# Kernel optimization log

Hardware: AMD Instinct MI355X
Metric: run time of the kernel (lower is better)

Reference implementation:

```python
import jax, jax.numpy as jnp
from jax import lax
import numpy as np

S, B, I, H, O = 65536, 1, 2, 128, 1


def setup_inputs() -> dict:
    key = jax.random.key(0)
    k1, k2, k3, k4 = jax.random.split(key, 4)
    # xavier_normal-style scales
    s_ih = (2.0 / (4 * H + I)) ** 0.5
    s_hh = (2.0 / (4 * H + H)) ** 0.5
    s_out = (2.0 / (H + O)) ** 0.5
    return {
        "x": jax.random.normal(k1, (S, B, I), jnp.float32),
        "h0": jnp.zeros((1, B, H), jnp.float32),
        "c0": jnp.zeros((1, B, H), jnp.float32),
        "W_ih": jax.random.normal(k2, (4 * H, I), jnp.float32) * s_ih,
        "W_hh": jax.random.normal(k3, (4 * H, H), jnp.float32) * s_hh,
        "b_ih": jnp.zeros((4 * H,), jnp.float32),
        "b_hh": jnp.zeros((4 * H,), jnp.float32),
        "W_out": jax.random.normal(k4, (O, H), jnp.float32) * s_out,
        "b_out": jnp.zeros((O,), jnp.float32),
    }


def reference(x, h0, c0, W_ih, W_hh, b_ih, b_hh, W_out, b_out):
    # Precompute input-to-gate projections for all timesteps: (S, B, 4H)
    xg = jnp.einsum("sbi,gi->sbg", x, W_ih) + b_ih + b_hh

    def step(carry, xg_t):
        h, c = carry  # (B, H) each
        gates = xg_t + h @ W_hh.T  # (B, 4H); PyTorch order i,f,g,o
        i, f, g, o = jnp.split(gates, 4, axis=-1)
        i = jax.nn.sigmoid(i)
        f = jax.nn.sigmoid(f)
        g = jnp.tanh(g)
        o = jax.nn.sigmoid(o)
        c = f * c + i * g
        h = o * jnp.tanh(c)
        return (h, c), h

    (_, _), hs = lax.scan(step, (h0[0], c0[0]), xg)  # hs: (S, B, H)
    out = jnp.tanh(hs.transpose(1, 0, 2))  # (B, S, H), matches permute(1,0,2)
    out = out @ W_out.T + b_out  # (B, S, O)
    return out.reshape(out.shape[0] * out.shape[1], -1)  # (B*S, O)
```

## Files before the change

kernel.cpp:

```cpp
#include <hip/hip_runtime.h>

#define S_LEN 65536
#define HDIM 128

typedef _Float16 half2_t __attribute__((ext_vector_type(2)));
typedef _Float16 half8_t __attribute__((ext_vector_type(8)));
typedef float f32x4 __attribute__((ext_vector_type(4)));

__device__ __forceinline__ float sigm(float x) {
    return 1.0f / (1.0f + __expf(-x));
}
__device__ __forceinline__ float tanh_fast(float x) {
    return 2.0f / (1.0f + __expf(-2.0f * x)) - 1.0f;
}
__device__ __forceinline__ float dot2(half2_t a, half2_t b, float c) {
#if __has_builtin(__builtin_amdgcn_fdot2)
    return __builtin_amdgcn_fdot2(a, b, c, false);
#else
    return fmaf((float)a.x, (float)b.x, fmaf((float)a.y, (float)b.y, c));
#endif
}

#define WG_BARRIER() do {                                         \
    asm volatile("s_waitcnt lgkmcnt(0)" ::: "memory");            \
    __builtin_amdgcn_s_barrier();                                 \
    asm volatile("" ::: "memory");                                \
} while (0)

__global__ __launch_bounds__(512)
__attribute__((amdgpu_waves_per_eu(2, 2)))
void lstm_seq_mfma(const float* __restrict__ x,
                   const float* __restrict__ h0,
                   const float* __restrict__ c0,
                   const float* __restrict__ W_ih,
                   const float* __restrict__ W_hh,
                   const float* __restrict__ b_ih,
                   const float* __restrict__ b_hh,
                   _Float16* __restrict__ h_hist)
{
    __shared__ __align__(16) _Float16 h_buf[2][HDIM];

    const int tid  = threadIdx.x;
    const int lane = tid & 63;
    const int w    = tid >> 6;
    const int m    = lane & 15;
    const int quad = lane >> 4;

#define LOAD_AF(i, cc) \
    half8_t af_##i##_##cc; { \
        const float* s_ = W_hh + (size_t)((i) * 128 + w * 16 + m) * HDIM \
                               + 32 * (cc) + 8 * quad; \
        af_##i##_##cc = (half8_t){ \
            (_Float16)s_[0], (_Float16)s_[1], (_Float16)s_[2], (_Float16)s_[3], \
            (_Float16)s_[4], (_Float16)s_[5], (_Float16)s_[6], (_Float16)s_[7] }; \
        asm volatile("" : "+v"(af_##i##_##cc)); }
    LOAD_AF(0, 0) LOAD_AF(0, 1) LOAD_AF(0, 2) LOAD_AF(0, 3)
    LOAD_AF(1, 0) LOAD_AF(1, 1) LOAD_AF(1, 2) LOAD_AF(1, 3)
    LOAD_AF(2, 0) LOAD_AF(2, 1) LOAD_AF(2, 2) LOAD_AF(2, 3)
    LOAD_AF(3, 0) LOAD_AF(3, 1) LOAD_AF(3, 2) LOAD_AF(3, 3)
#undef LOAD_AF

    const bool worker = (m < 4);
    const int  hidx   = w * 16 + quad * 4 + (m & 3);
    float wi00 = 0.f, wi01 = 0.f, bs0 = 0.f;
    float wi10 = 0.f, wi11 = 0.f, bs1 = 0.f;
    float wi20 = 0.f, wi21 = 0.f, bs2 = 0.f;
    float wi30 = 0.f, wi31 = 0.f, bs3 = 0.f;
    float c = 0.0f;
    if (worker) {
        const int r0 = hidx;
        const int r1 = hidx + 128;
        const int r2 = hidx + 256;
        const int r3 = hidx + 384;
        wi00 = W_ih[2 * r0]; wi01 = W_ih[2 * r0 + 1]; bs0 = b_ih[r0] + b_hh[r0];
        wi10 = W_ih[2 * r1]; wi11 = W_ih[2 * r1 + 1]; bs1 = b_ih[r1] + b_hh[r1];
        wi20 = W_ih[2 * r2]; wi21 = W_ih[2 * r2 + 1]; bs2 = b_ih[r2] + b_hh[r2];
        wi30 = W_ih[2 * r3]; wi31 = W_ih[2 * r3 + 1]; bs3 = b_ih[r3] + b_hh[r3];
        c = c0[hidx];
    }
    if (tid < HDIM) h_buf[0][tid] = (_Float16)h0[tid];
    __syncthreads();

    const float2* xp = (const float2*)x;
    float2 xcur = xp[0];
    float2 xn1  = xp[1];

    const bool selod = (m & 1) != 0;
    const bool selhi = (m & 2) != 0;

#define MFMA_T(i) \
    acc##i = __builtin_amdgcn_mfma_f32_16x16x32_f16(af_##i##_0, bf0, acc##i, 0, 0, 0); \
    acc##i = __builtin_amdgcn_mfma_f32_16x16x32_f16(af_##i##_1, bf1, acc##i, 0, 0, 0); \
    acc##i = __builtin_amdgcn_mfma_f32_16x16x32_f16(af_##i##_2, bf2, acc##i, 0, 0, 0); \
    acc##i = __builtin_amdgcn_mfma_f32_16x16x32_f16(af_##i##_3, bf3, acc##i, 0, 0, 0);

#define STEP(T, RB, WB) { \
     \
    const half8_t* hb_ = (const half8_t*)(RB); \
    half8_t bf0 = hb_[quad]; \
    half8_t bf1 = hb_[4 + quad]; \
    half8_t bf2 = hb_[8 + quad]; \
    half8_t bf3 = hb_[12 + quad]; \
    f32x4 acc0 = {0.f, 0.f, 0.f, 0.f}; \
    f32x4 acc1 = acc0, acc2 = acc0, acc3 = acc0; \
    MFMA_T(0) MFMA_T(1) MFMA_T(2) MFMA_T(3) \
    int tn_ = (T) + 2; if (tn_ >= S_LEN) tn_ = S_LEN - 1; \
    float2 xnew_ = xp[tn_]; \
    const float xg0 = fmaf(wi00, xcur.x, fmaf(wi01, xcur.y, bs0)); \
    const float xg1 = fmaf(wi10, xcur.x, fmaf(wi11, xcur.y, bs1)); \
    const float xg2 = fmaf(wi20, xcur.x, fmaf(wi21, xcur.y, bs2)); \
    const float xg3 = fmaf(wi30, xcur.x, fmaf(wi31, xcur.y, bs3)); \
    if (worker) { \
        float sa_, sb_; \
        sa_ = selod ? acc0[1] : acc0[0]; sb_ = selod ? acc0[3] : acc0[2]; \
        const float g0 = (selhi ? sb_ : sa_) + xg0; \
        sa_ = selod ? acc1[1] : acc1[0]; sb_ = selod ? acc1[3] : acc1[2]; \
        const float g1 = (selhi ? sb_ : sa_) + xg1; \
        sa_ = selod ? acc2[1] : acc2[0]; sb_ = selod ? acc2[3] : acc2[2]; \
        const float g2 = (selhi ? sb_ : sa_) + xg2; \
        sa_ = selod ? acc3[1] : acc3[0]; sb_ = selod ? acc3[3] : acc3[2]; \
        const float g3 = (selhi ? sb_ : sa_) + xg3; \
        const float gi = sigm(g0); \
        const float gf = sigm(g1); \
        const float gg = tanh_fast(g2); \
        const float go = sigm(g3); \
        c = fmaf(gf, c, gi * gg); \
        const float hv_ = go * tanh_fast(c); \
        const _Float16 hf_ = (_Float16)hv_; \
        (WB)[hidx] = hf_;                        \
        h_hist[(size_t)(T) * HDIM + hidx] = hf_;  \
    } \
    xcur = xn1; xn1 = xnew_; \
    WG_BARRIER(); }

    #pragma unroll 1
    for (int t = 0; t < S_LEN; t += 2) {
        STEP(t,     h_buf[0], h_buf[1])
        STEP(t + 1, h_buf[1], h_buf[0])
    }
#undef STEP
#undef MFMA_T
}

__global__ __launch_bounds__(256)
void out_proj(const _Float16* __restrict__ h_hist,
              const float* __restrict__ W_out,
              const float* __restrict__ b_out,
              float* __restrict__ out)
{
    const int lane  = threadIdx.x & 63;
    const int gwave = (blockIdx.x * 256 + threadIdx.x) >> 6;
    const int nwave = (gridDim.x * 256) >> 6;

    const float wo0 = W_out[2 * lane + 0];
    const float wo1 = W_out[2 * lane + 1];
    const float bout = b_out[0];

    for (int t = gwave; t < S_LEN; t += nwave) {
        half2_t hv = ((const half2_t*)(h_hist + t * HDIM))[lane];
        float p = tanh_fast((float)hv.x) * wo0 + tanh_fast((float)hv.y) * wo1;
        #pragma unroll
        for (int off = 32; off > 0; off >>= 1)
            p += __shfl_xor(p, off, 64);
        if (lane == 0) out[t] = p + bout;
    }
}

#define H_HI_OFF 144
__global__ __launch_bounds__(1024)
__attribute__((amdgpu_waves_per_eu(4, 4)))
void lstm_seq_full(const float* __restrict__ x,
                   const float* __restrict__ h0,
                   const float* __restrict__ c0,
                   const float* __restrict__ W_ih,
                   const float* __restrict__ W_hh,
                   const float* __restrict__ b_ih,
                   const float* __restrict__ b_hh,
                   const float* __restrict__ W_out,
                   const float* __restrict__ b_out,
                   float* __restrict__ out)
{
    __shared__ __align__(16) unsigned char h_raw[2 * H_HI_OFF];
    __shared__ float gates_part[2 * 512];
    __shared__ float red_sh[2];

    const int tid  = threadIdx.x;
    const int j    = tid >> 1;
    const int half = tid & 1;

    const float2* wr2 = (const float2*)(W_hh + j * HDIM + half * 64);
#define WDEF(i) half2_t W##i; { float2 t = wr2[i]; \
        W##i.x = (_Float16)t.x; W##i.y = (_Float16)t.y; } \
        asm volatile("" : "+v"(W##i));
    WDEF(0)  WDEF(1)  WDEF(2)  WDEF(3)  WDEF(4)  WDEF(5)  WDEF(6)  WDEF(7)
    WDEF(8)  WDEF(9)  WDEF(10) WDEF(11) WDEF(12) WDEF(13) WDEF(14) WDEF(15)
    WDEF(16) WDEF(17) WDEF(18) WDEF(19) WDEF(20) WDEF(21) WDEF(22) WDEF(23)
    WDEF(24) WDEF(25) WDEF(26) WDEF(27) WDEF(28) WDEF(29) WDEF(30) WDEF(31)
#undef WDEF

    float wih0 = 0.0f, wih1 = 0.0f, bias = 0.0f;
    if (half == 0) {
        wih0 = W_ih[2 * j + 0];
        wih1 = W_ih[2 * j + 1];
        bias = b_ih[j] + b_hh[j];
    }

    float c = 0.0f, wout = 0.0f;
    _Float16* hw = (_Float16*)(h_raw + ((tid < 64) ? 2 * tid
                                                   : H_HI_OFF + 2 * (tid - 64)));
    if (tid < HDIM) {
        c = c0[tid];
        wout = W_out[tid];
        *hw = (_Float16)h0[tid];
    }
    const float bout = b_out[0];
    __syncthreads();

    const float2* xp = (const float2*)x;
    float2 xcur = xp[0];
    const half8_t* hp = (const half8_t*)(h_raw + half * H_HI_OFF);

    #pragma unroll 1
    for (int t = 0; t < S_LEN; ++t) {
        const int tn = (t + 1 < S_LEN) ? (t + 1) : (S_LEN - 1);
        float2 xnext = xp[tn];

        float a0 = fmaf(wih0, xcur.x, fmaf(wih1, xcur.y, bias));
        float a1 = 0.0f, a2 = 0.0f, a3 = 0.0f;

#define CHUNK(cc, w0_, w1_, w2_, w3_) {                         \
        half8_t hv = hp[cc];                                    \
        half2_t p0 = { hv[0], hv[1] };                          \
        half2_t p1 = { hv[2], hv[3] };                          \
        half2_t p2 = { hv[4], hv[5] };                          \
        half2_t p3 = { hv[6], hv[7] };                          \
        a0 = dot2(w0_, p0, a0);                                 \
        a1 = dot2(w1_, p1, a1);                                 \
        a2 = dot2(w2_, p2, a2);                                 \
        a3 = dot2(w3_, p3, a3); }
        CHUNK(0, W0,  W1,  W2,  W3)
        CHUNK(1, W4,  W5,  W6,  W7)
        CHUNK(2, W8,  W9,  W10, W11)
        CHUNK(3, W12, W13, W14, W15)
        CHUNK(4, W16, W17, W18, W19)
        CHUNK(5, W20, W21, W22, W23)
        CHUNK(6, W24, W25, W26, W27)
        CHUNK(7, W28, W29, W30, W31)
#undef CHUNK

        gates_part[half * 512 + j] = (a0 + a1) + (a2 + a3);
        __syncthreads();

        if (tid < HDIM) {
            float gi = sigm(gates_part[tid]            + gates_part[tid + 512]);
            float gf = sigm(gates_part[tid + 128]      + gates_part[tid + 640]);
            float gg = tanh_fast(gates_part[tid + 256] + gates_part[tid + 768]);
            float go = sigm(gates_part[tid + 384]      + gates_part[tid + 896]);
            c = fmaf(gf, c, gi * gg);
            float h = go * tanh_fast(c);
            *hw = (_Float16)h;

            float p = tanh_fast(h) * wout;
            #pragma unroll
            for (int off = 32; off > 0; off >>= 1)
                p += __shfl_xor(p, off, 64);
            if ((tid & 63) == 0) red_sh[tid >> 6] = p;
        }
        __syncthreads();

        if (tid == 0) out[t] = red_sh[0] + red_sh[1] + bout;
        xcur = xnext;
    }
}

extern "C" void kernel_launch(void* const* d_in, const int* in_sizes, int n_in,
                              void* d_out, int out_size, void* d_ws, size_t ws_size,
                              hipStream_t stream) {
    const float* x     = (const float*)d_in[0];
    const float* h0    = (const float*)d_in[1];
    const float* c0    = (const float*)d_in[2];
    const float* W_ih  = (const float*)d_in[3];
    const float* W_hh  = (const float*)d_in[4];
    const float* b_ih  = (const float*)d_in[5];
    const float* b_hh  = (const float*)d_in[6];
    const float* W_out = (const float*)d_in[7];
    const float* b_out = (const float*)d_in[8];

    const size_t need = (size_t)S_LEN * HDIM * sizeof(_Float16);
    if (ws_size >= need) {
        _Float16* h_hist = (_Float16*)d_ws;
        lstm_seq_mfma<<<dim3(1), dim3(512), 0, stream>>>(
            x, h0, c0, W_ih, W_hh, b_ih, b_hh, h_hist);
        out_proj<<<dim3(1024), dim3(256), 0, stream>>>(
            h_hist, W_out, b_out, (float*)d_out);
    } else {
        lstm_seq_full<<<dim3(1), dim3(1024), 0, stream>>>(
            x, h0, c0, W_ih, W_hh, b_ih, b_hh, W_out, b_out, (float*)d_out);
    }
}
```

Before: 40.53 ms.

## Halve LSTM recurrence workgroup to four waves with two MFMA tiles each

The sequential LSTM kernel now runs with 256 threads (4 waves) instead of 512, and each wave computes two 16-row tiles per gate, holding twice as many W_hh fragments in registers. Gate selection picks among two tiles per gate, and eight lanes per 16 act as workers. Fewer waves should make the per-step workgroup barrier cheaper and cut cross-wave synchronization latency. The cost is twice the serial MFMA work and register pressure per wave. It also adds a pointer-increment history store and moves the x-projection FMAs ahead of the MFMAs.

```diff
diff --git a/kernel.cpp b/kernel.cpp
--- a/kernel.cpp
+++ b/kernel.cpp
@@ -27,8 +27,8 @@
     asm volatile("" ::: "memory");                                \
 } while (0)
 
-__global__ __launch_bounds__(512)
-__attribute__((amdgpu_waves_per_eu(2, 2)))
+__global__ __launch_bounds__(256)
+__attribute__((amdgpu_waves_per_eu(1, 1)))
 void lstm_seq_mfma(const float* __restrict__ x,
                    const float* __restrict__ h0,
                    const float* __restrict__ c0,
@@ -46,22 +46,26 @@
     const int m    = lane & 15;
     const int quad = lane >> 4;
 
-#define LOAD_AF(i, cc) \
-    half8_t af_##i##_##cc; { \
-        const float* s_ = W_hh + (size_t)((i) * 128 + w * 16 + m) * HDIM \
+#define LOAD_AF(i, ti, cc) \
+    half8_t af_##i##_##ti##_##cc; { \
+        const float* s_ = W_hh + (size_t)((i) * 128 + w * 32 + 16 * (ti) + m) * HDIM \
                                + 32 * (cc) + 8 * quad; \
-        af_##i##_##cc = (half8_t){ \
+        af_##i##_##ti##_##cc = (half8_t){ \
             (_Float16)s_[0], (_Float16)s_[1], (_Float16)s_[2], (_Float16)s_[3], \
             (_Float16)s_[4], (_Float16)s_[5], (_Float16)s_[6], (_Float16)s_[7] }; \
-        asm volatile("" : "+v"(af_##i##_##cc)); }
-    LOAD_AF(0, 0) LOAD_AF(0, 1) LOAD_AF(0, 2) LOAD_AF(0, 3)
-    LOAD_AF(1, 0) LOAD_AF(1, 1) LOAD_AF(1, 2) LOAD_AF(1, 3)
-    LOAD_AF(2, 0) LOAD_AF(2, 1) LOAD_AF(2, 2) LOAD_AF(2, 3)
-    LOAD_AF(3, 0) LOAD_AF(3, 1) LOAD_AF(3, 2) LOAD_AF(3, 3)
+        asm volatile("" : "+v"(af_##i##_##ti##_##cc)); }
+    LOAD_AF(0,0,0) LOAD_AF(0,0,1) LOAD_AF(0,0,2) LOAD_AF(0,0,3)
+    LOAD_AF(0,1,0) LOAD_AF(0,1,1) LOAD_AF(0,1,2) LOAD_AF(0,1,3)
+    LOAD_AF(1,0,0) LOAD_AF(1,0,1) LOAD_AF(1,0,2) LOAD_AF(1,0,3)
+    LOAD_AF(1,1,0) LOAD_AF(1,1,1) LOAD_AF(1,1,2) LOAD_AF(1,1,3)
+    LOAD_AF(2,0,0) LOAD_AF(2,0,1) LOAD_AF(2,0,2) LOAD_AF(2,0,3)
+    LOAD_AF(2,1,0) LOAD_AF(2,1,1) LOAD_AF(2,1,2) LOAD_AF(2,1,3)
+    LOAD_AF(3,0,0) LOAD_AF(3,0,1) LOAD_AF(3,0,2) LOAD_AF(3,0,3)
+    LOAD_AF(3,1,0) LOAD_AF(3,1,1) LOAD_AF(3,1,2) LOAD_AF(3,1,3)
 #undef LOAD_AF
 
-    const bool worker = (m < 4);
-    const int  hidx   = w * 16 + quad * 4 + (m & 3);
+    const bool worker = (m < 8);
+    const int  hidx   = w * 32 + 16 * ((m >> 2) & 1) + 4 * quad + (m & 3);
     float wi00 = 0.f, wi01 = 0.f, bs0 = 0.f;
     float wi10 = 0.f, wi11 = 0.f, bs1 = 0.f;
     float wi20 = 0.f, wi21 = 0.f, bs2 = 0.f;
@@ -87,39 +91,53 @@
 
     const bool selod = (m & 1) != 0;
     const bool selhi = (m & 2) != 0;
-
-#define MFMA_T(i) \
-    acc##i = __builtin_amdgcn_mfma_f32_16x16x32_f16(af_##i##_0, bf0, acc##i, 0, 0, 0); \
-    acc##i = __builtin_amdgcn_mfma_f32_16x16x32_f16(af_##i##_1, bf1, acc##i, 0, 0, 0); \
-    acc##i = __builtin_amdgcn_mfma_f32_16x16x32_f16(af_##i##_2, bf2, acc##i, 0, 0, 0); \
-    acc##i = __builtin_amdgcn_mfma_f32_16x16x32_f16(af_##i##_3, bf3, acc##i, 0, 0, 0);
-
-#define STEP(T, RB, WB) { \
+    const bool selti = (m & 4) != 0;
+
+    f32x4 zf = {0.f, 0.f, 0.f, 0.f};
+    asm volatile("" : "+v"(zf));
+
+    _Float16* hh = h_hist + hidx;
+
+#define MFMA_T(i, ti) \
+    f32x4 a_##i##_##ti; \
+    a_##i##_##ti = __builtin_amdgcn_mfma_f32_16x16x32_f16(af_##i##_##ti##_0, bf0, zf,           0, 0, 0); \
+    a_##i##_##ti = __builtin_amdgcn_mfma_f32_16x16x32_f16(af_##i##_##ti##_1, bf1, a_##i##_##ti, 0, 0, 0); \
+    a_##i##_##ti = __builtin_amdgcn_mfma_f32_16x16x32_f16(af_##i##_##ti##_2, bf2, a_##i##_##ti, 0, 0, 0); \
+    a_##i##_##ti = __builtin_amdgcn_mfma_f32_16x16x32_f16(af_##i##_##ti##_3, bf3, a_##i##_##ti, 0, 0, 0);
+
+#define GSEL(i, dst, xg_) { \
+    float lA_ = selod ? a_##i##_0[1] : a_##i##_0[0]; \
+    float hA_ = selod ? a_##i##_0[3] : a_##i##_0[2]; \
+    float vA_ = selhi ? hA_ : lA_; \
+    float lB_ = selod ? a_##i##_1[1] : a_##i##_1[0]; \
+    float hB_ = selod ? a_##i##_1[3] : a_##i##_1[2]; \
+    float vB_ = selhi ? hB_ : lB_; \
+    dst = (selti ? vB_ : vA_) + xg_; }
+
+#define STEP(T, RB, WB, OFF) { \
      \
     const half8_t* hb_ = (const half8_t*)(RB); \
     half8_t bf0 = hb_[quad]; \
     half8_t bf1 = hb_[4 + quad]; \
     half8_t bf2 = hb_[8 + quad]; \
     half8_t bf3 = hb_[12 + quad]; \
-    f32x4 acc0 = {0.f, 0.f, 0.f, 0.f}; \
-    f32x4 acc1 = acc0, acc2 = acc0, acc3 = acc0; \
-    MFMA_T(0) MFMA_T(1) MFMA_T(2) MFMA_T(3) \
     int tn_ = (T) + 2; if (tn_ >= S_LEN) tn_ = S_LEN - 1; \
     float2 xnew_ = xp[tn_]; \
+     \
     const float xg0 = fmaf(wi00, xcur.x, fmaf(wi01, xcur.y, bs0)); \
     const float xg1 = fmaf(wi10, xcur.x, fmaf(wi11, xcur.y, bs1)); \
     const float xg2 = fmaf(wi20, xcur.x, fmaf(wi21, xcur.y, bs2)); \
     const float xg3 = fmaf(wi30, xcur.x, fmaf(wi31, xcur.y, bs3)); \
+    MFMA_T(0, 0) MFMA_T(0, 1) \
+    MFMA_T(1, 0) MFMA_T(1, 1) \
+    MFMA_T(2, 0) MFMA_T(2, 1) \
+    MFMA_T(3, 0) MFMA_T(3, 1) \
     if (worker) { \
-        float sa_, sb_; \
-        sa_ = selod ? acc0[1] : acc0[0]; sb_ = selod ? acc0[3] : acc0[2]; \
-        const float g0 = (selhi ? sb_ : sa_) + xg0; \
-        sa_ = selod ? acc1[1] : acc1[0]; sb_ = selod ? acc1[3] : acc1[2]; \
-        const float g1 = (selhi ? sb_ : sa_) + xg1; \
-        sa_ = selod ? acc2[1] : acc2[0]; sb_ = selod ? acc2[3] : acc2[2]; \
-        const float g2 = (selhi ? sb_ : sa_) + xg2; \
-        sa_ = selod ? acc3[1] : acc3[0]; sb_ = selod ? acc3[3] : acc3[2]; \
-        const float g3 = (selhi ? sb_ : sa_) + xg3; \
+        float g0, g1, g2, g3; \
+        GSEL(0, g0, xg0) \
+        GSEL(1, g1, xg1) \
+        GSEL(2, g2, xg2) \
+        GSEL(3, g3, xg3) \
         const float gi = sigm(g0); \
         const float gf = sigm(g1); \
         const float gg = tanh_fast(g2); \
@@ -127,18 +145,20 @@
         c = fmaf(gf, c, gi * gg); \
         const float hv_ = go * tanh_fast(c); \
         const _Float16 hf_ = (_Float16)hv_; \
-        (WB)[hidx] = hf_;                        \
-        h_hist[(size_t)(T) * HDIM + hidx] = hf_;  \
+        (WB)[hidx] = hf_;                  \
+        hh[OFF] = hf_;                     \
     } \
     xcur = xn1; xn1 = xnew_; \
     WG_BARRIER(); }
 
     #pragma unroll 1
     for (int t = 0; t < S_LEN; t += 2) {
-        STEP(t,     h_buf[0], h_buf[1])
-        STEP(t + 1, h_buf[1], h_buf[0])
+        STEP(t,     h_buf[0], h_buf[1], 0)
+        STEP(t + 1, h_buf[1], h_buf[0], HDIM)
+        hh += 2 * HDIM;
     }
 #undef STEP
+#undef GSEL
 #undef MFMA_T
 }
 
@@ -289,7 +309,7 @@
     const size_t need = (size_t)S_LEN * HDIM * sizeof(_Float16);
     if (ws_size >= need) {
         _Float16* h_hist = (_Float16*)d_ws;
-        lstm_seq_mfma<<<dim3(1), dim3(512), 0, stream>>>(
+        lstm_seq_mfma<<<dim3(1), dim3(256), 0, stream>>>(
             x, h0, c0, W_ih, W_hh, b_ih, b_hh, h_hist);
         out_proj<<<dim3(1024), dim3(256), 0, stream>>>(
             h_hist, W_out, b_out, (float*)d_out);
```

After: 39.21 ms. 3.3% less time.

## Replace MFMA recurrent matvec with fdot2 dot products over 4 waves

Applied to the files above, without the earlier changes.

The sequential LSTM recurrence kernel drops the 16x16x32 MFMA formulation on 8 waves in favor of 4 waves. Each lane holds W_hh rows for one hidden unit across all four gates over half the K range and accumulates with packed fp16 dot2 instructions. A single xor-shuffle across the two wave halves combines the partial sums. The aim is to cut per-step latency on the serial critical path: MFMA issue and result latency, idle non-worker lanes, and the barrier cost across 8 waves. The trade-off is more VALU instructions per lane each step and heavier register pressure from the weights.

```diff
diff --git a/kernel.cpp b/kernel.cpp
--- a/kernel.cpp
+++ b/kernel.cpp
@@ -27,57 +27,56 @@
     asm volatile("" ::: "memory");                                \
 } while (0)
 
-__global__ __launch_bounds__(512)
-__attribute__((amdgpu_waves_per_eu(2, 2)))
-void lstm_seq_mfma(const float* __restrict__ x,
-                   const float* __restrict__ h0,
-                   const float* __restrict__ c0,
-                   const float* __restrict__ W_ih,
-                   const float* __restrict__ W_hh,
-                   const float* __restrict__ b_ih,
-                   const float* __restrict__ b_hh,
-                   _Float16* __restrict__ h_hist)
+__global__ __launch_bounds__(256)
+__attribute__((amdgpu_waves_per_eu(1, 1)))
+void lstm_seq_dot(const float* __restrict__ x,
+                  const float* __restrict__ h0,
+                  const float* __restrict__ c0,
+                  const float* __restrict__ W_ih,
+                  const float* __restrict__ W_hh,
+                  const float* __restrict__ b_ih,
+                  const float* __restrict__ b_hh,
+                  _Float16* __restrict__ h_hist)
 {
     __shared__ __align__(16) _Float16 h_buf[2][HDIM];
 
     const int tid  = threadIdx.x;
     const int lane = tid & 63;
     const int w    = tid >> 6;
-    const int m    = lane & 15;
-    const int quad = lane >> 4;
-
-#define LOAD_AF(i, cc) \
-    half8_t af_##i##_##cc; { \
-        const float* s_ = W_hh + (size_t)((i) * 128 + w * 16 + m) * HDIM \
-                               + 32 * (cc) + 8 * quad; \
-        af_##i##_##cc = (half8_t){ \
+    const int j    = lane & 31;
+    const int half = lane >> 5;
+    const int hidx = w * 32 + j;
+    const int k0   = half * 64;
+
+#define LOAD_WF(g, c) \
+    half8_t wf_##g##_##c; { \
+        const float* s_ = W_hh + (size_t)(hidx + 128 * (g)) * HDIM \
+                               + k0 + 8 * (c); \
+        wf_##g##_##c = (half8_t){ \
             (_Float16)s_[0], (_Float16)s_[1], (_Float16)s_[2], (_Float16)s_[3], \
             (_Float16)s_[4], (_Float16)s_[5], (_Float16)s_[6], (_Float16)s_[7] }; \
-        asm volatile("" : "+v"(af_##i##_##cc)); }
-    LOAD_AF(0, 0) LOAD_AF(0, 1) LOAD_AF(0, 2) LOAD_AF(0, 3)
-    LOAD_AF(1, 0) LOAD_AF(1, 1) LOAD_AF(1, 2) LOAD_AF(1, 3)
-    LOAD_AF(2, 0) LOAD_AF(2, 1) LOAD_AF(2, 2) LOAD_AF(2, 3)
-    LOAD_AF(3, 0) LOAD_AF(3, 1) LOAD_AF(3, 2) LOAD_AF(3, 3)
-#undef LOAD_AF
-
-    const bool worker = (m < 4);
-    const int  hidx   = w * 16 + quad * 4 + (m & 3);
-    float wi00 = 0.f, wi01 = 0.f, bs0 = 0.f;
-    float wi10 = 0.f, wi11 = 0.f, bs1 = 0.f;
-    float wi20 = 0.f, wi21 = 0.f, bs2 = 0.f;
-    float wi30 = 0.f, wi31 = 0.f, bs3 = 0.f;
-    float c = 0.0f;
-    if (worker) {
-        const int r0 = hidx;
-        const int r1 = hidx + 128;
-        const int r2 = hidx + 256;
-        const int r3 = hidx + 384;
-        wi00 = W_ih[2 * r0]; wi01 = W_ih[2 * r0 + 1]; bs0 = b_ih[r0] + b_hh[r0];
-        wi10 = W_ih[2 * r1]; wi11 = W_ih[2 * r1 + 1]; bs1 = b_ih[r1] + b_hh[r1];
-        wi20 = W_ih[2 * r2]; wi21 = W_ih[2 * r2 + 1]; bs2 = b_ih[r2] + b_hh[r2];
-        wi30 = W_ih[2 * r3]; wi31 = W_ih[2 * r3 + 1]; bs3 = b_ih[r3] + b_hh[r3];
-        c = c0[hidx];
-    }
+        asm volatile("" : "+v"(wf_##g##_##c)); }
+    LOAD_WF(0,0) LOAD_WF(0,1) LOAD_WF(0,2) LOAD_WF(0,3)
+    LOAD_WF(0,4) LOAD_WF(0,5) LOAD_WF(0,6) LOAD_WF(0,7)
+    LOAD_WF(1,0) LOAD_WF(1,1) LOAD_WF(1,2) LOAD_WF(1,3)
+    LOAD_WF(1,4) LOAD_WF(1,5) LOAD_WF(1,6) LOAD_WF(1,7)
+    LOAD_WF(2,0) LOAD_WF(2,1) LOAD_WF(2,2) LOAD_WF(2,3)
+    LOAD_WF(2,4) LOAD_WF(2,5) LOAD_WF(2,6) LOAD_WF(2,7)
+    LOAD_WF(3,0) LOAD_WF(3,1) LOAD_WF(3,2) LOAD_WF(3,3)
+    LOAD_WF(3,4) LOAD_WF(3,5) LOAD_WF(3,6) LOAD_WF(3,7)
+#undef LOAD_WF
+
+    const int r0 = hidx, r1 = hidx + 128, r2 = hidx + 256, r3 = hidx + 384;
+    const float wi00 = W_ih[2 * r0], wi01 = W_ih[2 * r0 + 1];
+    const float wi10 = W_ih[2 * r1], wi11 = W_ih[2 * r1 + 1];
+    const float wi20 = W_ih[2 * r2], wi21 = W_ih[2 * r2 + 1];
+    const float wi30 = W_ih[2 * r3], wi31 = W_ih[2 * r3 + 1];
+    const float bs0 = b_ih[r0] + b_hh[r0];
+    const float bs1 = b_ih[r1] + b_hh[r1];
+    const float bs2 = b_ih[r2] + b_hh[r2];
+    const float bs3 = b_ih[r3] + b_hh[r3];
+    float c = c0[hidx];
+
     if (tid < HDIM) h_buf[0][tid] = (_Float16)h0[tid];
     __syncthreads();
 
@@ -85,61 +84,76 @@
     float2 xcur = xp[0];
     float2 xn1  = xp[1];
 
-    const bool selod = (m & 1) != 0;
-    const bool selhi = (m & 2) != 0;
-
-#define MFMA_T(i) \
-    acc##i = __builtin_amdgcn_mfma_f32_16x16x32_f16(af_##i##_0, bf0, acc##i, 0, 0, 0); \
-    acc##i = __builtin_amdgcn_mfma_f32_16x16x32_f16(af_##i##_1, bf1, acc##i, 0, 0, 0); \
-    acc##i = __builtin_amdgcn_mfma_f32_16x16x32_f16(af_##i##_2, bf2, acc##i, 0, 0, 0); \
-    acc##i = __builtin_amdgcn_mfma_f32_16x16x32_f16(af_##i##_3, bf3, acc##i, 0, 0, 0);
-
-#define STEP(T, RB, WB) { \
+    const half8_t* hb0 = ((const half8_t*)h_buf[0]) + 8 * half;
+    const half8_t* hb1 = ((const half8_t*)h_buf[1]) + 8 * half;
+
+    _Float16* hh = h_hist + hidx;
+
+#define DOT8(acc, wv, hv) \
+    acc = dot2((half2_t){wv[0], wv[1]}, (half2_t){hv[0], hv[1]}, acc); \
+    acc = dot2((half2_t){wv[2], wv[3]}, (half2_t){hv[2], hv[3]}, acc); \
+    acc = dot2((half2_t){wv[4], wv[5]}, (half2_t){hv[4], hv[5]}, acc); \
+    acc = dot2((half2_t){wv[6], wv[7]}, (half2_t){hv[6], hv[7]}, acc);
+
+#define DCHUNK(a0_, a1_, a2_, a3_, c_, hv) \
+    DOT8(a0_, wf_0_##c_, hv) \
+    DOT8(a1_, wf_1_##c_, hv) \
+    DOT8(a2_, wf_2_##c_, hv) \
+    DOT8(a3_, wf_3_##c_, hv)
+
+#define STEP(T, RB, WB, OFF) { \
      \
-    const half8_t* hb_ = (const half8_t*)(RB); \
-    half8_t bf0 = hb_[quad]; \
-    half8_t bf1 = hb_[4 + quad]; \
-    half8_t bf2 = hb_[8 + quad]; \
-    half8_t bf3 = hb_[12 + quad]; \
-    f32x4 acc0 = {0.f, 0.f, 0.f, 0.f}; \
-    f32x4 acc1 = acc0, acc2 = acc0, acc3 = acc0; \
-    MFMA_T(0) MFMA_T(1) MFMA_T(2) MFMA_T(3) \
+    half8_t hv0 = (RB)[0], hv1 = (RB)[1], hv2 = (RB)[2], hv3 = (RB)[3]; \
+    half8_t hv4 = (RB)[4], hv5 = (RB)[5], hv6 = (RB)[6], hv7 = (RB)[7]; \
     int tn_ = (T) + 2; if (tn_ >= S_LEN) tn_ = S_LEN - 1; \
     float2 xnew_ = xp[tn_]; \
+     \
     const float xg0 = fmaf(wi00, xcur.x, fmaf(wi01, xcur.y, bs0)); \
     const float xg1 = fmaf(wi10, xcur.x, fmaf(wi11, xcur.y, bs1)); \
     const float xg2 = fmaf(wi20, xcur.x, fmaf(wi21, xcur.y, bs2)); \
     const float xg3 = fmaf(wi30, xcur.x, fmaf(wi31, xcur.y, bs3)); \
-    if (worker) { \
-        float sa_, sb_; \
-        sa_ = selod ? acc0[1] : acc0[0]; sb_ = selod ? acc0[3] : acc0[2]; \
-        const float g0 = (selhi ? sb_ : sa_) + xg0; \
-        sa_ = selod ? acc1[1] : acc1[0]; sb_ = selod ? acc1[3] : acc1[2]; \
-        const float g1 = (selhi ? sb_ : sa_) + xg1; \
-        sa_ = selod ? acc2[1] : acc2[0]; sb_ = selod ? acc2[3] : acc2[2]; \
-        const float g2 = (selhi ? sb_ : sa_) + xg2; \
-        sa_ = selod ? acc3[1] : acc3[0]; sb_ = selod ? acc3[3] : acc3[2]; \
-        const float g3 = (selhi ? sb_ : sa_) + xg3; \
-        const float gi = sigm(g0); \
-        const float gf = sigm(g1); \
-        const float gg = tanh_fast(g2); \
-        const float go = sigm(g3); \
-        c = fmaf(gf, c, gi * gg); \
-        const float hv_ = go * tanh_fast(c); \
-        const _Float16 hf_ = (_Float16)hv_; \
-        (WB)[hidx] = hf_;                        \
-        h_hist[(size_t)(T) * HDIM + hidx] = hf_;  \
+    float sA0 = 0.f, sA1 = 0.f, sA2 = 0.f, sA3 = 0.f; \
+    float sB0 = 0.f, sB1 = 0.f, sB2 = 0.f, sB3 = 0.f; \
+    DCHUNK(sA0, sA1, sA2, sA3, 0, hv0) \
+    DCHUNK(sB0, sB1, sB2, sB3, 1, hv1) \
+    DCHUNK(sA0, sA1, sA2, sA3, 2, hv2) \
+    DCHUNK(sB0, sB1, sB2, sB3, 3, hv3) \
+    DCHUNK(sA0, sA1, sA2, sA3, 4, hv4) \
+    DCHUNK(sB0, sB1, sB2, sB3, 5, hv5) \
+    DCHUNK(sA0, sA1, sA2, sA3, 6, hv6) \
+    DCHUNK(sB0, sB1, sB2, sB3, 7, hv7) \
+    float s0 = sA0 + sB0; \
+    float s1 = sA1 + sB1; \
+    float s2 = sA2 + sB2; \
+    float s3 = sA3 + sB3; \
+     \
+    s0 += __shfl_xor(s0, 32, 64); \
+    s1 += __shfl_xor(s1, 32, 64); \
+    s2 += __shfl_xor(s2, 32, 64); \
+    s3 += __shfl_xor(s3, 32, 64); \
+    const float gi = sigm(s0 + xg0); \
+    const float gf = sigm(s1 + xg1); \
+    const float gg = tanh_fast(s2 + xg2); \
+    const float go = sigm(s3 + xg3); \
+    c = fmaf(gf, c, gi * gg); \
+    const float hvx_ = go * tanh_fast(c); \
+    const _Float16 hf_ = (_Float16)hvx_; \
+    if (lane < 32) { \
+        (WB)[hidx] = hf_;                  \
+        hh[OFF] = hf_;                     \
     } \
     xcur = xn1; xn1 = xnew_; \
     WG_BARRIER(); }
 
     #pragma unroll 1
     for (int t = 0; t < S_LEN; t += 2) {
-        STEP(t,     h_buf[0], h_buf[1])
-        STEP(t + 1, h_buf[1], h_buf[0])
+        STEP(t,     hb0, h_buf[1], 0)
+        STEP(t + 1, hb1, h_buf[0], HDIM)
+        hh += 2 * HDIM;
     }
 #undef STEP
-#undef MFMA_T
+#undef DCHUNK
+#undef DOT8
 }
 
 __global__ __launch_bounds__(256)
@@ -289,7 +303,7 @@
     const size_t need = (size_t)S_LEN * HDIM * sizeof(_Float16);
     if (ws_size >= need) {
         _Float16* h_hist = (_Float16*)d_ws;
-        lstm_seq_mfma<<<dim3(1), dim3(512), 0, stream>>>(
+        lstm_seq_dot<<<dim3(1), dim3(256), 0, stream>>>(
             x, h0, c0, W_ih, W_hh, b_ih, b_hh, h_hist);
         out_proj<<<dim3(1024), dim3(256), 0, stream>>>(
             h_hist, W_out, b_out, (float*)d_out);
```

Result: no change. 41.27 ms (+1.8%).
